# Kernel optimization log

Hardware: AMD Instinct MI355X
Metric: run time of the kernel (lower is better)

## Reference

```python
import jax, jax.numpy as jnp
import numpy as np

# dims: L = 1 + H*W tokens (cls first), BT = B*T clips*frames
L, BT, D = 577, 128, 768
B, T = 16, 8
H = W = 24
CM = 192   # d_middle = D // REDUCTION(4)
CR = 48    # CM // rf_r(4)
K = 3      # rf_k and spatial kernel


def setup_inputs() -> dict:
    key = jax.random.key(0)
    ks = jax.random.split(key, 10)
    return {
        "x":      jax.random.normal(ks[0], (L, BT, D), jnp.float32),
        # tada_pre_proj: Linear(D -> CM)
        "w_pre":  jax.random.normal(ks[1], (D, CM), jnp.float32) * 0.02,
        "b_pre":  jnp.zeros((CM,), jnp.float32),
        # TAdaConv2dV2 base depthwise weight (1x3x3, groups=CM) and bias
        "w_base": jax.random.normal(ks[2], (K, K, 1, CM), jnp.float32) * 0.1,
        "b_conv": jnp.zeros((CM,), jnp.float32),
        # route function: global 1x1 branch, temporal conv a (CM->CR), temporal conv b (CR->CM, small init)
        "w_g":    jax.random.normal(ks[3], (CM, CM), jnp.float32) * 0.02,
        "b_g":    jnp.zeros((CM,), jnp.float32),
        "w_a":    jax.random.normal(ks[4], (K, CM, CR), jnp.float32) * 0.05,
        "b_a":    jnp.zeros((CR,), jnp.float32),
        "w_b":    jax.random.normal(ks[5], (K, CR, CM), jnp.float32) * 0.02,
        # tada_proj: Linear(CM -> D)
        "w_proj": jax.random.normal(ks[6], (CM, D), jnp.float32) * 0.02,
        "b_proj": jnp.zeros((D,), jnp.float32),
    }


def reference(x, w_pre, b_pre, w_base, b_conv, w_g, b_g, w_a, b_a, w_b, w_proj, b_proj):
    # --- tada_pre_proj ---
    h = x @ w_pre + b_pre                                   # [L, BT, CM]
    cls_tok, sp = h[:1], h[1:]                              # cls token bypasses the conv
    sp = sp.transpose(1, 0, 2).reshape(BT, H, W, CM)        # [BT, H, W, CM]

    # --- route function: per-frame, per-channel calibration alpha ---
    d = sp.reshape(B, T, H * W, CM).mean(axis=2)            # spatial avg pool -> [B, T, CM]
    g = d.mean(axis=1) @ w_g + b_g                          # global temporal descriptor [B, CM]
    a = jax.lax.conv_general_dilated(d + g[:, None, :], w_a, (1,), 'SAME',
                                     dimension_numbers=('NWC', 'WIO', 'NWC')) + b_a
    a = jax.nn.relu(a)                                      # [B, T, CR]
    alpha = jax.lax.conv_general_dilated(a, w_b, (1,), 'SAME',
                                         dimension_numbers=('NWC', 'WIO', 'NWC')) + 1.0  # [B, T, CM]

    # --- calibrated depthwise conv (cal_dim='cout') ---
    # conv2d(x, alpha * W_base) == alpha * conv2d(x, W_base) for depthwise cout calibration
    y = jax.lax.conv_general_dilated(sp, w_base, (1, 1), 'SAME',
                                     dimension_numbers=('NHWC', 'HWIO', 'NHWC'),
                                     feature_group_count=CM)
    y = y * alpha.reshape(BT, 1, 1, CM) + b_conv            # [BT, H, W, CM]
    y = y.reshape(BT, H * W, CM).transpose(1, 0, 2)         # [HW, BT, CM]
    out = jnp.concatenate([cls_tok, y], axis=0)             # [L, BT, CM]

    # --- QuickGELU + tada_proj ---
    out = out * jax.nn.sigmoid(1.702 * out)
    return out @ w_proj + b_proj                            # [L, BT, D]
```

## Files before the change

### kernel.cpp

```cpp
#include <hip/hip_runtime.h>

#define DEV __device__ __forceinline__

typedef short bf16x8 __attribute__((ext_vector_type(8)));
typedef float f32x4  __attribute__((ext_vector_type(4)));


DEV unsigned short f2bf(float f) {
  unsigned u = __float_as_uint(f);
  unsigned r = (u + 0x7fffu + ((u >> 16) & 1u)) >> 16;
  return (unsigned short)r;
}

DEV unsigned cvt_pk_bf16(float a, float b) {
  unsigned r;
  asm("v_cvt_pk_bf16_f32 %0, %1, %2" : "=v"(r) : "v"(a), "v"(b));
  return r;
}

DEV float bf2f(unsigned short b) { return __uint_as_float((unsigned)b << 16); }

DEV float silu_g(float v) { return v / (1.f + __expf(-1.702f * v)); }

DEV void gload_lds16(const void* g, void* l) {
  __builtin_amdgcn_global_load_lds(
      (const __attribute__((address_space(1))) unsigned int*)g,
      (__attribute__((address_space(3))) unsigned int*)l, 16, 0, 0);
}

__global__ __launch_bounds__(256)
void prep_kernel(const float* __restrict__ w_pre, const float* __restrict__ w_proj,
                 short* __restrict__ w_preT, short* __restrict__ w_projT) {
  int i = blockIdx.x * 256 + threadIdx.x;
  if (i < 192 * 768) {
    int n = i / 768, k = i - n * 768;
    w_preT[i] = (short)f2bf(w_pre[k * 192 + n]);
    int n2 = i / 192, k2 = i - n2 * 192;
    w_projT[i] = (short)f2bf(w_proj[k2 * 768 + n2]);
  }
}

template<bool A_BF16, int KTOT, int NTOT, bool NT_STORE>
__global__ __launch_bounds__(512)
void gemm_kernel(const void* __restrict__ A_, const short* __restrict__ Bt,
                 const float* __restrict__ bias, float* __restrict__ C) {
  constexpr int BM = 128, BN = 192, BK = 64;
  __shared__ short As[BM * BK];
  __shared__ short Bs[BN * BK];

  const int tid  = threadIdx.x;
  const int wave = tid >> 6, lane = tid & 63;
  const int m0 = blockIdx.x * BM;
  const int n0 = blockIdx.y * BN;
  const int wm = wave >> 2, wn = wave & 3;
  const int lr  = lane & 15;
  const int lk8 = lane >> 4;
  const int srow = lane >> 3;
  const int schunk = lane & 7;

  const float* Af = (const float*)A_;
  const short* Ab = (const short*)A_;

  f32x4 acc[4][3] = {};
  float4 areg[2][2];

  auto loadA_f32 = [&](int kt) {
    #pragma unroll
    for (int s = 0; s < 2; ++s) {
      int id = tid + s * 512;
      int r = id >> 3, c = id & 7;
      int cg = c ^ (r & 7);
      const float* p = Af + (size_t)(m0 + r) * KTOT + kt + cg * 8;
      areg[s][0] = *(const float4*)p;
      areg[s][1] = *(const float4*)(p + 4);
    }
  };

  if constexpr (!A_BF16) loadA_f32(0);

  for (int kt = 0; kt < KTOT; kt += BK) {
    if constexpr (A_BF16) {
      #pragma unroll
      for (int j = 0; j < 2; ++j) {
        int rb8 = wave * 2 + j;
        int r = rb8 * 8 + srow;
        int cg = schunk ^ (srow);
        const short* src = Ab + (size_t)(m0 + r) * KTOT + kt + cg * 8;
        gload_lds16(src, (char*)As + rb8 * 1024);
      }
    } else {
      #pragma unroll
      for (int s = 0; s < 2; ++s) {
        int id = tid + s * 512;
        int r = id >> 3, c = id & 7;
        int4 w;
        w.x = (int)cvt_pk_bf16(areg[s][0].x, areg[s][0].y);
        w.y = (int)cvt_pk_bf16(areg[s][0].z, areg[s][0].w);
        w.z = (int)cvt_pk_bf16(areg[s][1].x, areg[s][1].y);
        w.w = (int)cvt_pk_bf16(areg[s][1].z, areg[s][1].w);
        *(int4*)&As[r * 64 + c * 8] = w;
      }
    }
    #pragma unroll
    for (int j = 0; j < 3; ++j) {
      int rb8 = wave * 3 + j;
      int r = rb8 * 8 + srow;
      int cg = schunk ^ (srow);
      const short* src = Bt + (size_t)(n0 + r) * KTOT + kt + cg * 8;
      gload_lds16(src, (char*)Bs + rb8 * 1024);
    }
    __syncthreads();

    if constexpr (!A_BF16) {
      if (kt + BK < KTOT) loadA_f32(kt + BK);
    }

    #pragma unroll
    for (int ks = 0; ks < 2; ++ks) {
      int kc = ks * 4 + lk8;
      bf16x8 af[4], bfv[3];
      #pragma unroll
      for (int fm = 0; fm < 4; ++fm) {
        int row = wm * 64 + fm * 16 + lr;
        af[fm] = *(const bf16x8*)&As[row * 64 + (kc ^ (row & 7)) * 8];
      }
      #pragma unroll
      for (int fn = 0; fn < 3; ++fn) {
        int row = wn * 48 + fn * 16 + lr;
        bfv[fn] = *(const bf16x8*)&Bs[row * 64 + (kc ^ (row & 7)) * 8];
      }
      #pragma unroll
      for (int fm = 0; fm < 4; ++fm)
        #pragma unroll
        for (int fn = 0; fn < 3; ++fn)
          acc[fm][fn] = __builtin_amdgcn_mfma_f32_16x16x32_bf16(
              bfv[fn], af[fm], acc[fm][fn], 0, 0, 0);
    }
    __syncthreads();
  }

  const int cb = (lane >> 4) * 4;
  #pragma unroll
  for (int fm = 0; fm < 4; ++fm) {
    int row = m0 + wm * 64 + fm * 16 + lr;
    #pragma unroll
    for (int fn = 0; fn < 3; ++fn) {
      int col = n0 + wn * 48 + fn * 16 + cb;
      float4 bv = *(const float4*)(bias + col);
      f32x4 o;
      o[0] = acc[fm][fn][0] + bv.x;
      o[1] = acc[fm][fn][1] + bv.y;
      o[2] = acc[fm][fn][2] + bv.z;
      o[3] = acc[fm][fn][3] + bv.w;
      f32x4* dst = (f32x4*)&C[(size_t)row * NTOT + col];
      if constexpr (NT_STORE) __builtin_nontemporal_store(o, dst);
      else                    *dst = o;
    }
  }
}

__global__ __launch_bounds__(192)
void reduce_d_kernel(const float* __restrict__ h, float* __restrict__ dpart) {
  int bt = blockIdx.x, chunk = blockIdx.y, c = threadIdx.x;
  int l0 = 1 + chunk * 144;
  float sum = 0.f;
  #pragma unroll 8
  for (int i = 0; i < 144; ++i)
    sum += h[(size_t)((l0 + i) * 128 + bt) * 192 + c];
  dpart[(size_t)(chunk * 128 + bt) * 192 + c] = sum * (1.f / 576.f);
}

__global__ __launch_bounds__(256)
void small_path_kernel(const float* __restrict__ dpart,
                       const float* __restrict__ w_g, const float* __restrict__ b_g,
                       const float* __restrict__ w_a, const float* __restrict__ b_a,
                       const float* __restrict__ w_b,
                       float* __restrict__ alpha) {
  const int b = blockIdx.x, tid = threadIdx.x;
  __shared__ unsigned short wbuf[36864];
  __shared__ float e[8][192];
  __shared__ float md[192];
  __shared__ float a[8][48];

  #pragma unroll
  for (int it = 0; it < 36; ++it) {
    int i = tid + it * 256;
    float4 v = *(const float4*)(w_g + i * 4);
    int2 w;
    w.x = (int)cvt_pk_bf16(v.x, v.y);
    w.y = (int)cvt_pk_bf16(v.z, v.w);
    *(int2*)&wbuf[i * 4] = w;
  }
  {
    const float4* dp4 = (const float4*)dpart;
    for (int i = tid; i < 384; i += 256) {
      float4 v0 = dp4[b * 384 + i];
      float4 v1 = dp4[6144 + b * 384 + i];
      float4 v2 = dp4[12288 + b * 384 + i];
      float4 v3 = dp4[18432 + b * 384 + i];
      float4 v;
      v.x = (v0.x + v1.x) + (v2.x + v3.x);
      v.y = (v0.y + v1.y) + (v2.y + v3.y);
      v.z = (v0.z + v1.z) + (v2.z + v3.z);
      v.w = (v0.w + v1.w) + (v2.w + v3.w);
      *(float4*)((float*)e + i * 4) = v;
    }
  }
  __syncthreads();

  if (tid < 192) {
    float m = 0.f;
    #pragma unroll
    for (int t = 0; t < 8; ++t) m += e[t][tid];
    md[tid] = m * 0.125f;
  }
  __syncthreads();

  if (tid < 192) {
    float accg = b_g[tid];
    #pragma unroll 8
    for (int k = 0; k < 192; ++k)
      accg += md[k] * bf2f(wbuf[k * 192 + tid]);
    #pragma unroll
    for (int t = 0; t < 8; ++t) e[t][tid] += accg;
  }
  __syncthreads();

  #pragma unroll
  for (int it = 0; it < 27; ++it) {
    int i = tid + it * 256;
    float4 v = *(const float4*)(w_a + i * 4);
    int2 w;
    w.x = (int)cvt_pk_bf16(v.x, v.y);
    w.y = (int)cvt_pk_bf16(v.z, v.w);
    *(int2*)&wbuf[i * 4] = w;
  }
  __syncthreads();

  for (int o = tid; o < 384; o += 256) {
    int t = o / 48, r = o - t * 48;
    float acc = b_a[r];
    #pragma unroll
    for (int dt = 0; dt < 3; ++dt) {
      int tt = t + dt - 1;
      if ((unsigned)tt < 8u) {
        #pragma unroll 8
        for (int k = 0; k < 192; ++k)
          acc += e[tt][k] * bf2f(wbuf[(dt * 192 + k) * 48 + r]);
      }
    }
    a[t][r] = fmaxf(acc, 0.f);
  }
  __syncthreads();

  #pragma unroll
  for (int it = 0; it < 27; ++it) {
    int i = tid + it * 256;
    float4 v = *(const float4*)(w_b + i * 4);
    int2 w;
    w.x = (int)cvt_pk_bf16(v.x, v.y);
    w.y = (int)cvt_pk_bf16(v.z, v.w);
    *(int2*)&wbuf[i * 4] = w;
  }
  __syncthreads();

  if (tid < 192) {
    #pragma unroll
    for (int t = 0; t < 8; ++t) {
      float acc = 1.0f;
      #pragma unroll
      for (int dt = 0; dt < 3; ++dt) {
        int tt = t + dt - 1;
        if ((unsigned)tt < 8u) {
          #pragma unroll 8
          for (int r = 0; r < 48; ++r)
            acc += a[tt][r] * bf2f(wbuf[(dt * 48 + r) * 192 + tid]);
        }
      }
      alpha[(size_t)(b * 8 + t) * 192 + tid] = acc;
    }
  }
}

__global__ __launch_bounds__(256)
void dwconv_silu_kernel(const float* __restrict__ h, const float* __restrict__ alpha,
                        const float* __restrict__ w_base, const float* __restrict__ b_conv,
                        unsigned short* __restrict__ s) {
  const int bt = blockIdx.x, c0 = blockIdx.y * 32;
  const int tid = threadIdx.x;
  __shared__ float tile[576][32];

  #pragma unroll
  for (int it = 0; it < 18; ++it) {
    int gidx = tid + it * 256;
    int p = gidx >> 3, cc = (gidx & 7) * 4;
    *(float4*)&tile[p][cc] =
        *(const float4*)(h + (size_t)((1 + p) * 128 + bt) * 192 + c0 + cc);
  }

  const int c = tid & 31;
  const int prow = tid >> 5;
  float wv[3][3];
  #pragma unroll
  for (int dh = 0; dh < 3; ++dh)
    #pragma unroll
    for (int dw = 0; dw < 3; ++dw)
      wv[dh][dw] = w_base[(dh * 3 + dw) * 192 + c0 + c];
  const float av = alpha[bt * 192 + c0 + c];
  const float bc = b_conv[c0 + c];

  if (tid < 32) {
    float v = h[(size_t)bt * 192 + c0 + tid];
    s[(size_t)bt * 192 + c0 + tid] = f2bf(silu_g(v));
  }
  __syncthreads();

  for (int i = 0; i < 72; ++i) {
    int p = prow + i * 8;
    int hh = p / 24, ww = p - hh * 24;
    float acc = 0.f;
    #pragma unroll
    for (int dh = 0; dh < 3; ++dh) {
      int y = hh + dh - 1;
      if ((unsigned)y >= 24u) continue;
      #pragma unroll
      for (int dw = 0; dw < 3; ++dw) {
        int xx = ww + dw - 1;
        if ((unsigned)xx >= 24u) continue;
        acc += tile[y * 24 + xx][c] * wv[dh][dw];
      }
    }
    float pre = acc * av + bc;
    s[(size_t)((1 + p) * 128 + bt) * 192 + c0 + c] = f2bf(silu_g(pre));
  }
}

extern "C" void kernel_launch(void* const* d_in, const int* in_sizes, int n_in,
                              void* d_out, int out_size, void* d_ws, size_t ws_size,
                              hipStream_t stream) {
  (void)in_sizes; (void)n_in; (void)out_size; (void)ws_size;
  const float* x      = (const float*)d_in[0];
  const float* w_pre  = (const float*)d_in[1];
  const float* b_pre  = (const float*)d_in[2];
  const float* w_base = (const float*)d_in[3];
  const float* b_conv = (const float*)d_in[4];
  const float* w_g    = (const float*)d_in[5];
  const float* b_g    = (const float*)d_in[6];
  const float* w_a    = (const float*)d_in[7];
  const float* b_a    = (const float*)d_in[8];
  const float* w_b    = (const float*)d_in[9];
  const float* w_proj = (const float*)d_in[10];
  const float* b_proj = (const float*)d_in[11];

  float* out = (float*)d_out;
  float* h   = (float*)d_out;
  char* ws = (char*)d_ws;
  short* w_preT  = (short*)(ws);
  short* w_projT = (short*)(ws + 294912);
  float* dbuf    = (float*)(ws + 589824);
  float* alpha   = (float*)(ws + 983040);
  short* s       = (short*)(ws + 1081344);

  prep_kernel<<<576, 256, 0, stream>>>(w_pre, w_proj, w_preT, w_projT);

  gemm_kernel<false, 768, 192, false><<<dim3(577, 1), 512, 0, stream>>>(
      x, w_preT, b_pre, h);

  reduce_d_kernel<<<dim3(128, 4), 192, 0, stream>>>(h, dbuf);
  small_path_kernel<<<16, 256, 0, stream>>>(dbuf, w_g, b_g, w_a, b_a, w_b, alpha);
  dwconv_silu_kernel<<<dim3(128, 6), 256, 0, stream>>>(h, alpha, w_base, b_conv,
                                                       (unsigned short*)s);

  gemm_kernel<true, 192, 768, true><<<dim3(577, 4), 512, 0, stream>>>(
      s, w_projT, b_proj, out);
}
```

Before: 292.6 us.

## Store intermediate h in bf16, double-buffer GEMM LDS, single-pass spatial reduction

The first GEMM now writes its hidden activation in bf16 rather than fp32, which halves the traffic for h in the reduction and depthwise-conv kernels. The GEMM kernel gains double-buffered LDS tiles, so the loads for the next K-slice overlap the MFMAs on the current one, at the cost of twice the shared memory. The reduce kernel now does the full 576-token reduction per frame in one block using bf16x8 loads, which removes the partial-sum buffer and the combine step in small_path. Rounding h to bf16 adds precision loss to the pooled mean and the conv input.

Result: faster. 247.1 us (-15.5%).

```diff
diff --git a/kernel.cpp b/kernel.cpp
--- a/kernel.cpp
+++ b/kernel.cpp
@@ -4,6 +4,7 @@
 
 typedef short bf16x8 __attribute__((ext_vector_type(8)));
 typedef float f32x4  __attribute__((ext_vector_type(4)));
+typedef unsigned short ushort_t;
 
 
 DEV unsigned short f2bf(float f) {
@@ -40,13 +41,14 @@
   }
 }
 
-template<bool A_BF16, int KTOT, int NTOT, bool NT_STORE>
-__global__ __launch_bounds__(512)
+template<bool A_BF16, int KTOT, int NTOT, bool OUT_BF16, bool NT_STORE>
+__global__ __launch_bounds__(512, 4)
 void gemm_kernel(const void* __restrict__ A_, const short* __restrict__ Bt,
-                 const float* __restrict__ bias, float* __restrict__ C) {
+                 const float* __restrict__ bias, void* __restrict__ C_) {
   constexpr int BM = 128, BN = 192, BK = 64;
-  __shared__ short As[BM * BK];
-  __shared__ short Bs[BN * BK];
+  constexpr int NT = KTOT / BK;
+  __shared__ short As[2][BM * BK];
+  __shared__ short Bs[2][BN * BK];
 
   const int tid  = threadIdx.x;
   const int wave = tid >> 6, lane = tid & 63;
@@ -75,46 +77,38 @@
       areg[s][1] = *(const float4*)(p + 4);
     }
   };
-
-  if constexpr (!A_BF16) loadA_f32(0);
-
-  for (int kt = 0; kt < KTOT; kt += BK) {
-    if constexpr (A_BF16) {
-      #pragma unroll
-      for (int j = 0; j < 2; ++j) {
-        int rb8 = wave * 2 + j;
-        int r = rb8 * 8 + srow;
-        int cg = schunk ^ (srow);
-        const short* src = Ab + (size_t)(m0 + r) * KTOT + kt + cg * 8;
-        gload_lds16(src, (char*)As + rb8 * 1024);
-      }
-    } else {
-      #pragma unroll
-      for (int s = 0; s < 2; ++s) {
-        int id = tid + s * 512;
-        int r = id >> 3, c = id & 7;
-        int4 w;
-        w.x = (int)cvt_pk_bf16(areg[s][0].x, areg[s][0].y);
-        w.y = (int)cvt_pk_bf16(areg[s][0].z, areg[s][0].w);
-        w.z = (int)cvt_pk_bf16(areg[s][1].x, areg[s][1].y);
-        w.w = (int)cvt_pk_bf16(areg[s][1].z, areg[s][1].w);
-        *(int4*)&As[r * 64 + c * 8] = w;
-      }
-    }
+  auto cvtStoreA = [&](int buf) {
+    #pragma unroll
+    for (int s = 0; s < 2; ++s) {
+      int id = tid + s * 512;
+      int r = id >> 3, c = id & 7;
+      int4 w;
+      w.x = (int)cvt_pk_bf16(areg[s][0].x, areg[s][0].y);
+      w.y = (int)cvt_pk_bf16(areg[s][0].z, areg[s][0].w);
+      w.z = (int)cvt_pk_bf16(areg[s][1].x, areg[s][1].y);
+      w.w = (int)cvt_pk_bf16(areg[s][1].z, areg[s][1].w);
+      *(int4*)&As[buf][r * 64 + c * 8] = w;
+    }
+  };
+  auto stageA16 = [&](int kt, int buf) {
+    #pragma unroll
+    for (int j = 0; j < 2; ++j) {
+      int rb8 = wave * 2 + j;
+      int r = rb8 * 8 + srow;
+      const short* src = Ab + (size_t)(m0 + r) * KTOT + kt + (schunk ^ srow) * 8;
+      gload_lds16(src, (char*)As[buf] + rb8 * 1024);
+    }
+  };
+  auto stageB = [&](int kt, int buf) {
     #pragma unroll
     for (int j = 0; j < 3; ++j) {
       int rb8 = wave * 3 + j;
       int r = rb8 * 8 + srow;
-      int cg = schunk ^ (srow);
-      const short* src = Bt + (size_t)(n0 + r) * KTOT + kt + cg * 8;
-      gload_lds16(src, (char*)Bs + rb8 * 1024);
-    }
-    __syncthreads();
-
-    if constexpr (!A_BF16) {
-      if (kt + BK < KTOT) loadA_f32(kt + BK);
-    }
-
+      const short* src = Bt + (size_t)(n0 + r) * KTOT + kt + (schunk ^ srow) * 8;
+      gload_lds16(src, (char*)Bs[buf] + rb8 * 1024);
+    }
+  };
+  auto compute = [&](int buf) {
     #pragma unroll
     for (int ks = 0; ks < 2; ++ks) {
       int kc = ks * 4 + lk8;
@@ -122,12 +116,12 @@
       #pragma unroll
       for (int fm = 0; fm < 4; ++fm) {
         int row = wm * 64 + fm * 16 + lr;
-        af[fm] = *(const bf16x8*)&As[row * 64 + (kc ^ (row & 7)) * 8];
+        af[fm] = *(const bf16x8*)&As[buf][row * 64 + (kc ^ (row & 7)) * 8];
       }
       #pragma unroll
       for (int fn = 0; fn < 3; ++fn) {
         int row = wn * 48 + fn * 16 + lr;
-        bfv[fn] = *(const bf16x8*)&Bs[row * 64 + (kc ^ (row & 7)) * 8];
+        bfv[fn] = *(const bf16x8*)&Bs[buf][row * 64 + (kc ^ (row & 7)) * 8];
       }
       #pragma unroll
       for (int fm = 0; fm < 4; ++fm)
@@ -136,7 +130,28 @@
           acc[fm][fn] = __builtin_amdgcn_mfma_f32_16x16x32_bf16(
               bfv[fn], af[fm], acc[fm][fn], 0, 0, 0);
     }
-    __syncthreads();
+  };
+
+  if constexpr (!A_BF16) { loadA_f32(0); cvtStoreA(0); }
+  else                   stageA16(0, 0);
+  stageB(0, 0);
+  if constexpr (!A_BF16) { if (NT > 1) loadA_f32(BK); }
+  __syncthreads();
+
+  #pragma unroll
+  for (int t = 0; t < NT; ++t) {
+    const int cur = t & 1, nxt = cur ^ 1;
+    if (t + 1 < NT) {
+      if constexpr (!A_BF16) {
+        cvtStoreA(nxt);
+        if (t + 2 < NT) loadA_f32((t + 2) * BK);
+      } else {
+        stageA16((t + 1) * BK, nxt);
+      }
+      stageB((t + 1) * BK, nxt);
+    }
+    compute(cur);
+    if (t + 1 < NT) __syncthreads();
   }
 
   const int cb = (lane >> 4) * 4;
@@ -147,31 +162,51 @@
     for (int fn = 0; fn < 3; ++fn) {
       int col = n0 + wn * 48 + fn * 16 + cb;
       float4 bv = *(const float4*)(bias + col);
-      f32x4 o;
-      o[0] = acc[fm][fn][0] + bv.x;
-      o[1] = acc[fm][fn][1] + bv.y;
-      o[2] = acc[fm][fn][2] + bv.z;
-      o[3] = acc[fm][fn][3] + bv.w;
-      f32x4* dst = (f32x4*)&C[(size_t)row * NTOT + col];
-      if constexpr (NT_STORE) __builtin_nontemporal_store(o, dst);
-      else                    *dst = o;
+      float o0 = acc[fm][fn][0] + bv.x;
+      float o1 = acc[fm][fn][1] + bv.y;
+      float o2 = acc[fm][fn][2] + bv.z;
+      float o3 = acc[fm][fn][3] + bv.w;
+      if constexpr (OUT_BF16) {
+        ushort_t* Cb = (ushort_t*)C_;
+        int2 w;
+        w.x = (int)cvt_pk_bf16(o0, o1);
+        w.y = (int)cvt_pk_bf16(o2, o3);
+        *(int2*)&Cb[(size_t)row * NTOT + col] = w;
+      } else {
+        float* Cf = (float*)C_;
+        f32x4 o; o[0] = o0; o[1] = o1; o[2] = o2; o[3] = o3;
+        f32x4* dst = (f32x4*)&Cf[(size_t)row * NTOT + col];
+        if constexpr (NT_STORE) __builtin_nontemporal_store(o, dst);
+        else                    *dst = o;
+      }
     }
   }
 }
 
 __global__ __launch_bounds__(192)
-void reduce_d_kernel(const float* __restrict__ h, float* __restrict__ dpart) {
-  int bt = blockIdx.x, chunk = blockIdx.y, c = threadIdx.x;
-  int l0 = 1 + chunk * 144;
-  float sum = 0.f;
-  #pragma unroll 8
-  for (int i = 0; i < 144; ++i)
-    sum += h[(size_t)((l0 + i) * 128 + bt) * 192 + c];
-  dpart[(size_t)(chunk * 128 + bt) * 192 + c] = sum * (1.f / 576.f);
+void reduce_d_kernel(const ushort_t* __restrict__ h, float* __restrict__ d) {
+  const int bt = blockIdx.x, tid = threadIdx.x;
+  const int slice = tid / 24, c8 = tid % 24;
+  __shared__ float part[8][192];
+  float sum[8] = {};
+  #pragma unroll 4
+  for (int i = 0; i < 72; ++i) {
+    int l = 1 + slice * 72 + i;
+    bf16x8 v = *(const bf16x8*)&h[((size_t)l * 128 + bt) * 192 + c8 * 8];
+    #pragma unroll
+    for (int j = 0; j < 8; ++j) sum[j] += bf2f((unsigned short)v[j]);
+  }
+  #pragma unroll
+  for (int j = 0; j < 8; ++j) part[slice][c8 * 8 + j] = sum[j];
+  __syncthreads();
+  float s = 0.f;
+  #pragma unroll
+  for (int sl = 0; sl < 8; ++sl) s += part[sl][tid];
+  d[bt * 192 + tid] = s * (1.f / 576.f);
 }
 
 __global__ __launch_bounds__(256)
-void small_path_kernel(const float* __restrict__ dpart,
+void small_path_kernel(const float* __restrict__ d,
                        const float* __restrict__ w_g, const float* __restrict__ b_g,
                        const float* __restrict__ w_a, const float* __restrict__ b_a,
                        const float* __restrict__ w_b,
@@ -191,21 +226,8 @@
     w.y = (int)cvt_pk_bf16(v.z, v.w);
     *(int2*)&wbuf[i * 4] = w;
   }
-  {
-    const float4* dp4 = (const float4*)dpart;
-    for (int i = tid; i < 384; i += 256) {
-      float4 v0 = dp4[b * 384 + i];
-      float4 v1 = dp4[6144 + b * 384 + i];
-      float4 v2 = dp4[12288 + b * 384 + i];
-      float4 v3 = dp4[18432 + b * 384 + i];
-      float4 v;
-      v.x = (v0.x + v1.x) + (v2.x + v3.x);
-      v.y = (v0.y + v1.y) + (v2.y + v3.y);
-      v.z = (v0.z + v1.z) + (v2.z + v3.z);
-      v.w = (v0.w + v1.w) + (v2.w + v3.w);
-      *(float4*)((float*)e + i * 4) = v;
-    }
-  }
+  for (int i = tid; i < 384; i += 256)
+    *(float4*)((float*)e + i * 4) = *(const float4*)(d + (size_t)b * 1536 + i * 4);
   __syncthreads();
 
   if (tid < 192) {
@@ -283,19 +305,19 @@
 }
 
 __global__ __launch_bounds__(256)
-void dwconv_silu_kernel(const float* __restrict__ h, const float* __restrict__ alpha,
+void dwconv_silu_kernel(const ushort_t* __restrict__ h, const float* __restrict__ alpha,
                         const float* __restrict__ w_base, const float* __restrict__ b_conv,
-                        unsigned short* __restrict__ s) {
+                        ushort_t* __restrict__ s) {
   const int bt = blockIdx.x, c0 = blockIdx.y * 32;
   const int tid = threadIdx.x;
-  __shared__ float tile[576][32];
-
-  #pragma unroll
-  for (int it = 0; it < 18; ++it) {
+  __shared__ ushort_t tile[576][32];
+
+  #pragma unroll
+  for (int it = 0; it < 9; ++it) {
     int gidx = tid + it * 256;
-    int p = gidx >> 3, cc = (gidx & 7) * 4;
-    *(float4*)&tile[p][cc] =
-        *(const float4*)(h + (size_t)((1 + p) * 128 + bt) * 192 + c0 + cc);
+    int p = gidx >> 2, cc = (gidx & 3) * 8;
+    *(bf16x8*)&tile[p][cc] =
+        *(const bf16x8*)&h[((size_t)(1 + p) * 128 + bt) * 192 + c0 + cc];
   }
 
   const int c = tid & 31;
@@ -310,7 +332,7 @@
   const float bc = b_conv[c0 + c];
 
   if (tid < 32) {
-    float v = h[(size_t)bt * 192 + c0 + tid];
+    float v = bf2f(h[(size_t)bt * 192 + c0 + tid]);
     s[(size_t)bt * 192 + c0 + tid] = f2bf(silu_g(v));
   }
   __syncthreads();
@@ -327,7 +349,7 @@
       for (int dw = 0; dw < 3; ++dw) {
         int xx = ww + dw - 1;
         if ((unsigned)xx >= 24u) continue;
-        acc += tile[y * 24 + xx][c] * wv[dh][dw];
+        acc += bf2f(tile[y * 24 + xx][c]) * wv[dh][dw];
       }
     }
     float pre = acc * av + bc;
@@ -353,24 +375,24 @@
   const float* b_proj = (const float*)d_in[11];
 
   float* out = (float*)d_out;
-  float* h   = (float*)d_out;
+  ushort_t* h = (ushort_t*)d_out;
   char* ws = (char*)d_ws;
   short* w_preT  = (short*)(ws);
   short* w_projT = (short*)(ws + 294912);
   float* dbuf    = (float*)(ws + 589824);
-  float* alpha   = (float*)(ws + 983040);
-  short* s       = (short*)(ws + 1081344);
+  float* alpha   = (float*)(ws + 688128);
+  short* s       = (short*)(ws + 786432);
 
   prep_kernel<<<576, 256, 0, stream>>>(w_pre, w_proj, w_preT, w_projT);
 
-  gemm_kernel<false, 768, 192, false><<<dim3(577, 1), 512, 0, stream>>>(
+  gemm_kernel<false, 768, 192, true, false><<<dim3(577, 1), 512, 0, stream>>>(
       x, w_preT, b_pre, h);
 
-  reduce_d_kernel<<<dim3(128, 4), 192, 0, stream>>>(h, dbuf);
+  reduce_d_kernel<<<128, 192, 0, stream>>>(h, dbuf);
   small_path_kernel<<<16, 256, 0, stream>>>(dbuf, w_g, b_g, w_a, b_a, w_b, alpha);
   dwconv_silu_kernel<<<dim3(128, 6), 256, 0, stream>>>(h, alpha, w_base, b_conv,
-                                                       (unsigned short*)s);
-
-  gemm_kernel<true, 192, 768, true><<<dim3(577, 4), 512, 0, stream>>>(
+                                                       (ushort_t*)s);
+
+  gemm_kernel<true, 192, 768, false, true><<<dim3(577, 4), 512, 0, stream>>>(
       s, w_projT, b_proj, out);
 }
```
